# Optimization experiments

Hardware: AMD Instinct MI355X
Metric: run time of the kernel (lower is better)

Reference implementation:

```python
import jax, jax.numpy as jnp
import numpy as np

EPS = 1e-5  # torch LayerNorm default

def _layernorm(x, g, b):
    mu = jnp.mean(x, axis=-1, keepdims=True)
    var = jnp.mean(jnp.square(x - mu), axis=-1, keepdims=True)
    return (x - mu) * jax.lax.rsqrt(var + EPS) * g + b

def _gelu(x):
    return jax.nn.gelu(x, approximate=False)  # torch nn.GELU default is exact erf

def setup_inputs() -> dict:
    B, S, D, F = 2, 128, 64, 256
    key = jax.random.key(0)
    ks = jax.random.split(key, 8)
    def xavier(k, fan_in, fan_out, gain=1.0):
        lim = gain * np.sqrt(6.0 / (fan_in + fan_out))
        return jax.random.uniform(k, (fan_in, fan_out), jnp.float32, -lim, lim)
    return {
        "q": jax.random.normal(ks[0], (B, S, D), jnp.float32),
        # gauge generator MLP: Linear(2D, F) -> GELU -> Linear(F, D*D)
        "gw1": xavier(ks[1], 2 * D, F),
        "gb1": jnp.zeros((F,), jnp.float32),
        "gw2": xavier(ks[2], F, D * D, gain=0.01),  # nn.init.xavier_uniform_(gain=0.01)
        "gb2": jnp.zeros((D * D,), jnp.float32),    # nn.init.zeros_
        # block MLP: Linear(D, F) -> GELU -> Linear(F, D)
        "mw1": xavier(ks[3], D, F),
        "mb1": jnp.zeros((F,), jnp.float32),
        "mw2": xavier(ks[4], F, D),
        "mb2": jnp.zeros((D,), jnp.float32),
        # LayerNorms
        "ln1_g": jnp.ones((D,), jnp.float32),
        "ln1_b": jnp.zeros((D,), jnp.float32),
        "ln2_g": jnp.ones((D,), jnp.float32),
        "ln2_b": jnp.zeros((D,), jnp.float32),
    }

def reference(q, gw1, gb1, gw2, gb2, mw1, mb1, mw2, mb2, ln1_g, ln1_b, ln2_g, ln2_b):
    B, S, D = q.shape
    phi = q
    # pairwise features: cat(phi_i, phi_j) -> (B, S, S, 2D)
    phi_i = jnp.broadcast_to(phi[:, :, None, :], (B, S, S, D))
    phi_j = jnp.broadcast_to(phi[:, None, :, :], (B, S, S, D))
    pairs = jnp.concatenate([phi_i, phi_j], axis=-1)
    # gauge MLP -> U_ij in (B, S, S, D, D)
    h = _gelu(pairs @ gw1 + gb1)
    U = (h @ gw2 + gb2).reshape(B, S, S, D, D)
    # aggregate: sum_j U_ij @ phi_j  (contract d with phi feature dim)
    agg = jnp.einsum('bijde,bjd->bie', U, phi)
    # dropout in eval mode = identity
    phi = _layernorm(phi + agg, ln1_g, ln1_b)
    mlp_out = _gelu(phi @ mw1 + mb1) @ mw2 + mb2
    return _layernorm(phi + mlp_out, ln2_g, ln2_b)
```

## Files before the change

kernel.cpp:

```cpp
#include <hip/hip_runtime.h>
#include <hip/hip_bf16.h>
#include <math.h>

namespace {

constexpr int NB = 2, NS = 128, ND = 64, NF = 256;

typedef __attribute__((ext_vector_type(8))) short short8;
typedef __attribute__((ext_vector_type(8))) unsigned short ushort8;
typedef __attribute__((ext_vector_type(4))) float floatx4;

constexpr size_t OFF_W2   = 0;
constexpr size_t SZ_W2    = (size_t)NB * NS * NF * ND;
constexpr size_t OFF_P    = OFF_W2 + SZ_W2;
constexpr size_t SZ_P     = (size_t)NB * NS * NS * ND;
constexpr size_t OFF_AT   = OFF_P + SZ_P;
constexpr size_t SZ_AT    = (size_t)NB * NF * NS;
constexpr size_t OFF_BT   = OFF_AT + SZ_AT;
constexpr size_t SZ_BT    = (size_t)NB * NS * NF;
constexpr size_t OFF_BIAS = OFF_BT + SZ_BT;

__device__ __forceinline__ float gelu_fast(float x) {
  const float xs = fabsf(x) * 0.70710678118654752f;
  const float t = __builtin_amdgcn_rcpf(fmaf(0.3275911f, xs, 1.0f));
  float p = fmaf(1.061405429f, t, -1.453152027f);
  p = fmaf(p, t, 1.421413741f);
  p = fmaf(p, t, -0.284496736f);
  p = fmaf(p, t, 0.254829592f);
  p *= t;
  const float e = __expf(-xs * xs);
  const float erf_ax = fmaf(-p, e, 1.0f);
  const float erf_x = copysignf(erf_ax, x);
  return 0.5f * x * (1.0f + erf_x);
}

constexpr int QT_LD = NS + 4;

__global__ __launch_bounds__(256) void kA_pre(const float* __restrict__ q,
                                              const float* __restrict__ gw1,
                                              const float* __restrict__ gb1,
                                              const float* __restrict__ gw2,
                                              const float* __restrict__ gb2,
                                              float* __restrict__ A_t,
                                              float* __restrict__ Bt,
                                              float* __restrict__ W2,
                                              float* __restrict__ bias_agg) {
  __shared__ __align__(16) float smem[ND * QT_LD + ND * ND];
  const int t = threadIdx.x;
  const int bid = blockIdx.x;
  if (bid < NB * NS) {
    const int b = bid / NS, i = bid % NS;
    float* qrow = smem;
    if (t < ND) qrow[t] = q[((size_t)b * NS + i) * ND + t];
    __syncthreads();
    const int f = t;
    float a = 0.f, bb = gb1[f];
    #pragma unroll 8
    for (int d = 0; d < ND; ++d) {
      const float qd = qrow[d];
      a  += qd * gw1[d * NF + f];
      bb += qd * gw1[(ND + d) * NF + f];
    }
    A_t[((size_t)b * NF + f) * NS + i] = a;
    Bt[((size_t)b * NS + i) * NF + f] = bb;
  } else if (bid < NB * NS + NB * NF) {
    const int idx = bid - NB * NS;
    const int b = idx / NF, f = idx % NF;
    float* qt = smem;
    float* G  = smem + ND * QT_LD;
    for (int r = 0; r < ND * ND / 256; ++r)
      G[t + r * 256] = gw2[(size_t)f * ND * ND + t + r * 256];
    const float* qb = q + (size_t)b * NS * ND;
    for (int r = 0; r < NS * ND / 256; ++r) {
      const int lin = t + r * 256;
      const int j = lin >> 6, d = lin & 63;
      qt[d * QT_LD + j] = qb[lin];
    }
    __syncthreads();
    const int tj = t >> 3, te = t & 7;
    const int j0 = tj * 4, e0 = te * 8;
    float acc[4][8];
    #pragma unroll
    for (int jj = 0; jj < 4; ++jj)
      #pragma unroll
      for (int ee = 0; ee < 8; ++ee) acc[jj][ee] = 0.f;
    #pragma unroll 4
    for (int d = 0; d < ND; ++d) {
      const float4 qv = *(const float4*)&qt[d * QT_LD + j0];
      const float4 g0 = *(const float4*)&G[d * ND + e0];
      const float4 g1 = *(const float4*)&G[d * ND + e0 + 4];
      const float qa[4] = {qv.x, qv.y, qv.z, qv.w};
      const float ga[8] = {g0.x, g0.y, g0.z, g0.w, g1.x, g1.y, g1.z, g1.w};
      #pragma unroll
      for (int jj = 0; jj < 4; ++jj)
        #pragma unroll
        for (int ee = 0; ee < 8; ++ee) acc[jj][ee] += qa[jj] * ga[ee];
    }
    #pragma unroll
    for (int jj = 0; jj < 4; ++jj) {
      const int j = j0 + jj;
      float* dst = W2 + (((size_t)b * NS + j) * NF + f) * ND + e0;
      *(float4*)&dst[0] = make_float4(acc[jj][0], acc[jj][1], acc[jj][2], acc[jj][3]);
      *(float4*)&dst[4] = make_float4(acc[jj][4], acc[jj][5], acc[jj][6], acc[jj][7]);
    }
  } else {
    const int b = bid - (NB * NS + NB * NF);
    float* qs = smem;
    float* colsum = smem + NS * ND;
    const float* qb = q + (size_t)b * NS * ND;
    for (int r = 0; r < NS * ND / 256; ++r) qs[t + r * 256] = qb[t + r * 256];
    __syncthreads();
    if (t < ND) {
      float s = 0.f;
      for (int j = 0; j < NS; ++j) s += qs[j * ND + t];
      colsum[t] = s;
    }
    __syncthreads();
    if (t < ND) {
      float acc = 0.f;
      for (int d = 0; d < ND; ++d) acc += gb2[d * ND + t] * colsum[d];
      bias_agg[b * ND + t] = acc;
    }
  }
}

constexpr int HLD = 72;

__global__ __launch_bounds__(512) void k2_main(const float* __restrict__ A_t,
                                               const float* __restrict__ Bt,
                                               const float* __restrict__ W2,
                                               float* __restrict__ P) {
  const int b = blockIdx.x / NS, j = blockIdx.x % NS;
  const int t = threadIdx.x;
  const int lane = t & 63, w = t >> 6;
  __shared__ float Btj[NF];
  __shared__ __align__(16) unsigned short Hc[NS * HLD];
  __shared__ __align__(16) unsigned short Wc[ND * HLD];
  if (t < NF) Btj[t] = Bt[((size_t)b * NS + j) * NF + t];

  const float* W2bj = W2 + ((size_t)b * NS + j) * NF * ND;
  const float* Ab = A_t + (size_t)b * NF * NS;

  const int wi = (w & 3) * 32, we = (w >> 2) * 32;
  const int m = lane & 15, quad = lane >> 4;

  const int hi = (w & 1) * 64 + lane;
  const int hoct0 = t >> 7;
  const int weid = t & 63, woct = t >> 6;

  floatx4 acc[2][2];
  #pragma unroll
  for (int a0 = 0; a0 < 2; ++a0)
    #pragma unroll
    for (int a1 = 0; a1 < 2; ++a1) acc[a0][a1] = (floatx4)0.f;

  for (int c = 0; c < NF / 64; ++c) {
    __syncthreads();
    float wv[8];
    #pragma unroll
    for (int r = 0; r < 8; ++r)
      wv[r] = W2bj[(size_t)(c * 64 + woct * 8 + r) * ND + weid];
    float hv[2][8];
    #pragma unroll
    for (int s = 0; s < 2; ++s) {
      const int oct = hoct0 + 4 * s;
      #pragma unroll
      for (int r = 0; r < 8; ++r) {
        const int f = c * 64 + oct * 8 + r;
        hv[s][r] = gelu_fast(Ab[(size_t)f * NS + hi] + Btj[f]);
      }
    }
    {
      union { __hip_bfloat162 b2[4]; ushort8 v; } u;
      #pragma unroll
      for (int p = 0; p < 4; ++p)
        u.b2[p] = __float22bfloat162_rn(make_float2(wv[2 * p], wv[2 * p + 1]));
      *(ushort8*)&Wc[weid * HLD + woct * 8] = u.v;
    }
    #pragma unroll
    for (int s = 0; s < 2; ++s) {
      union { __hip_bfloat162 b2[4]; ushort8 v; } u;
      #pragma unroll
      for (int p = 0; p < 4; ++p)
        u.b2[p] = __float22bfloat162_rn(make_float2(hv[s][2 * p], hv[s][2 * p + 1]));
      *(ushort8*)&Hc[hi * HLD + (hoct0 + 4 * s) * 8] = u.v;
    }
    __syncthreads();
    #pragma unroll
    for (int kk = 0; kk < 2; ++kk) {
      short8 afr[2], bfr[2];
      #pragma unroll
      for (int ti = 0; ti < 2; ++ti)
        afr[ti] = *(const short8*)&Hc[(wi + ti * 16 + m) * HLD + kk * 32 + quad * 8];
      #pragma unroll
      for (int te = 0; te < 2; ++te)
        bfr[te] = *(const short8*)&Wc[(we + te * 16 + m) * HLD + kk * 32 + quad * 8];
      #pragma unroll
      for (int ti = 0; ti < 2; ++ti)
        #pragma unroll
        for (int te = 0; te < 2; ++te)
          acc[ti][te] = __builtin_amdgcn_mfma_f32_16x16x32_bf16(
              afr[ti], bfr[te], acc[ti][te], 0, 0, 0);
    }
  }
  float* Pbj = P + ((size_t)b * NS + j) * NS * ND;
  #pragma unroll
  for (int ti = 0; ti < 2; ++ti)
    #pragma unroll
    for (int te = 0; te < 2; ++te)
      #pragma unroll
      for (int r = 0; r < 4; ++r) {
        const int row = wi + ti * 16 + quad * 4 + r;
        const int col = we + te * 16 + m;
        Pbj[(size_t)row * ND + col] = acc[ti][te][r];
      }
}

__global__ __launch_bounds__(512) void k3_epi(const float* __restrict__ q,
                                              const float* __restrict__ P,
                                              const float* __restrict__ bias_agg,
                                              const float* __restrict__ mw1,
                                              const float* __restrict__ mb1,
                                              const float* __restrict__ mw2,
                                              const float* __restrict__ mb2,
                                              const float* __restrict__ ln1g,
                                              const float* __restrict__ ln1b,
                                              const float* __restrict__ ln2g,
                                              const float* __restrict__ ln2b,
                                              float* __restrict__ out) {
  const int b = blockIdx.x / NS, i = blockIdx.x % NS;
  const int t = threadIdx.x;
  const int e = t & 63, g = t >> 6;
  __shared__ float red[8 * ND];
  __shared__ float phi1[ND];
  __shared__ float hid[NF];
  const float* Pb = P + (size_t)b * NS * NS * ND;
  float s = 0.f;
  #pragma unroll 4
  for (int m0 = 0; m0 < 16; ++m0) {
    const int jj = g * 16 + m0;
    s += Pb[((size_t)jj * NS + i) * ND + e];
  }
  red[t] = s;
  __syncthreads();
  if (t < ND) {
    float agg = bias_agg[b * ND + e];
    #pragma unroll
    for (int gg = 0; gg < 8; ++gg) agg += red[gg * ND + e];
    const float x = q[((size_t)b * NS + i) * ND + e] + agg;
    float sum = x, sumsq = x * x;
    #pragma unroll
    for (int off = 32; off >= 1; off >>= 1) {
      sum += __shfl_xor(sum, off);
      sumsq += __shfl_xor(sumsq, off);
    }
    const float mu = sum * (1.f / 64.f);
    const float var = sumsq * (1.f / 64.f) - mu * mu;
    const float inv = rsqrtf(var + 1e-5f);
    phi1[e] = (x - mu) * inv * ln1g[e] + ln1b[e];
  }
  __syncthreads();
  if (t < NF) {
    float h = mb1[t];
    #pragma unroll 8
    for (int d = 0; d < ND; ++d) h += phi1[d] * mw1[d * NF + t];
    hid[t] = gelu_fast(h);
  }
  __syncthreads();
  {
    float p = 0.f;
    #pragma unroll 8
    for (int m0 = 0; m0 < 32; ++m0) {
      const int f = g * 32 + m0;
      p += hid[f] * mw2[f * ND + e];
    }
    red[t] = p;
  }
  __syncthreads();
  if (t < ND) {
    float mlp = mb2[e];
    #pragma unroll
    for (int gg = 0; gg < 8; ++gg) mlp += red[gg * ND + e];
    const float x = phi1[e] + mlp;
    float sum = x, sumsq = x * x;
    #pragma unroll
    for (int off = 32; off >= 1; off >>= 1) {
      sum += __shfl_xor(sum, off);
      sumsq += __shfl_xor(sumsq, off);
    }
    const float mu = sum * (1.f / 64.f);
    const float var = sumsq * (1.f / 64.f) - mu * mu;
    const float inv = rsqrtf(var + 1e-5f);
    out[((size_t)b * NS + i) * ND + e] = (x - mu) * inv * ln2g[e] + ln2b[e];
  }
}

}

extern "C" void kernel_launch(void* const* d_in, const int* in_sizes, int n_in,
                              void* d_out, int out_size, void* d_ws, size_t ws_size,
                              hipStream_t stream) {
  const float* q    = (const float*)d_in[0];
  const float* gw1  = (const float*)d_in[1];
  const float* gb1  = (const float*)d_in[2];
  const float* gw2  = (const float*)d_in[3];
  const float* gb2  = (const float*)d_in[4];
  const float* mw1  = (const float*)d_in[5];
  const float* mb1  = (const float*)d_in[6];
  const float* mw2  = (const float*)d_in[7];
  const float* mb2  = (const float*)d_in[8];
  const float* ln1g = (const float*)d_in[9];
  const float* ln1b = (const float*)d_in[10];
  const float* ln2g = (const float*)d_in[11];
  const float* ln2b = (const float*)d_in[12];
  float* out = (float*)d_out;
  float* ws  = (float*)d_ws;

  float* W2   = ws + OFF_W2;
  float* Pp   = ws + OFF_P;
  float* A_t  = ws + OFF_AT;
  float* Bt   = ws + OFF_BT;
  float* bias = ws + OFF_BIAS;

  kA_pre<<<NB * NS + NB * NF + NB, 256, 0, stream>>>(q, gw1, gb1, gw2, gb2,
                                                     A_t, Bt, W2, bias);
  k2_main<<<NB * NS, 512, 0, stream>>>(A_t, Bt, W2, Pp);
  k3_epi<<<NB * NS, 512, 0, stream>>>(q, Pp, bias, mw1, mb1, mw2, mb2,
                                      ln1g, ln1b, ln2g, ln2b, out);
}
```

Before: 112.9 us.

## Store W2 intermediate in bf16, compute it with MFMA, and prefetch in main loop

The precompute of W2 (q contracted with gw2 per feature) now runs on bf16 MFMA instructions with swizzled shared-memory tiles and writes a bf16 intermediate instead of fp32. That halves the global traffic for the largest workspace tensor, both on write and on read in the main kernel. The main kernel also register-prefetches the next chunk's W2 and A_t values before the barrier, so global loads overlap with compute, and the precompute blocks are regrouped with 512 threads each. The trade-off is an extra bf16 rounding of q and gw2 before the product is formed, plus scalar 2-byte output stores.

```diff
diff --git a/kernel.cpp b/kernel.cpp
--- a/kernel.cpp
+++ b/kernel.cpp
@@ -10,9 +10,9 @@
 typedef __attribute__((ext_vector_type(8))) unsigned short ushort8;
 typedef __attribute__((ext_vector_type(4))) float floatx4;
 
-constexpr size_t OFF_W2   = 0;
-constexpr size_t SZ_W2    = (size_t)NB * NS * NF * ND;
-constexpr size_t OFF_P    = OFF_W2 + SZ_W2;
+constexpr size_t OFF_W2H  = 0;
+constexpr size_t SZ_W2H   = (size_t)NB * NS * NF * ND / 2;
+constexpr size_t OFF_P    = OFF_W2H + SZ_W2H;
 constexpr size_t SZ_P     = (size_t)NB * NS * NS * ND;
 constexpr size_t OFF_AT   = OFF_P + SZ_P;
 constexpr size_t SZ_AT    = (size_t)NB * NF * NS;
@@ -34,92 +34,124 @@
   return 0.5f * x * (1.0f + erf_x);
 }
 
-constexpr int QT_LD = NS + 4;
-
-__global__ __launch_bounds__(256) void kA_pre(const float* __restrict__ q,
+__device__ __forceinline__ ushort8 pack_bf16x8(const float v[8]) {
+  union { __hip_bfloat162 b2[4]; ushort8 u; } u;
+  #pragma unroll
+  for (int p = 0; p < 4; ++p)
+    u.b2[p] = __float22bfloat162_rn(make_float2(v[2 * p], v[2 * p + 1]));
+  return u.u;
+}
+
+__global__ __launch_bounds__(512) void kA_pre(const float* __restrict__ q,
                                               const float* __restrict__ gw1,
                                               const float* __restrict__ gb1,
                                               const float* __restrict__ gw2,
                                               const float* __restrict__ gb2,
                                               float* __restrict__ A_t,
                                               float* __restrict__ Bt,
-                                              float* __restrict__ W2,
+                                              unsigned short* __restrict__ W2h,
                                               float* __restrict__ bias_agg) {
-  __shared__ __align__(16) float smem[ND * QT_LD + ND * ND];
-  const int t = threadIdx.x;
-  const int bid = blockIdx.x;
-  if (bid < NB * NS) {
-    const int b = bid / NS, i = bid % NS;
-    float* qrow = smem;
-    if (t < ND) qrow[t] = q[((size_t)b * NS + i) * ND + t];
+  __shared__ __align__(16) unsigned short smem_u[128 * 64 + 8 * 64 * 40];
+  float* smf = (float*)smem_u;
+  const int t = threadIdx.x, bid = blockIdx.x;
+
+  if (bid < 128) {
+    const int b = bid >> 6, ip = bid & 63;
+    const int half = t >> 8, f = t & 255;
+    const int i = ip * 2 + half;
+    float* qrow = smf;
+    if (f < 64) qrow[half * 64 + f] = q[((size_t)b * NS + i) * ND + f];
     __syncthreads();
-    const int f = t;
     float a = 0.f, bb = gb1[f];
     #pragma unroll 8
     for (int d = 0; d < ND; ++d) {
-      const float qd = qrow[d];
+      const float qd = qrow[half * 64 + d];
       a  += qd * gw1[d * NF + f];
       bb += qd * gw1[(ND + d) * NF + f];
     }
     A_t[((size_t)b * NF + f) * NS + i] = a;
     Bt[((size_t)b * NS + i) * NF + f] = bb;
-  } else if (bid < NB * NS + NB * NF) {
-    const int idx = bid - NB * NS;
-    const int b = idx / NF, f = idx % NF;
-    float* qt = smem;
-    float* G  = smem + ND * QT_LD;
-    for (int r = 0; r < ND * ND / 256; ++r)
-      G[t + r * 256] = gw2[(size_t)f * ND * ND + t + r * 256];
-    const float* qb = q + (size_t)b * NS * ND;
-    for (int r = 0; r < NS * ND / 256; ++r) {
-      const int lin = t + r * 256;
-      const int j = lin >> 6, d = lin & 63;
-      qt[d * QT_LD + j] = qb[lin];
-    }
-    __syncthreads();
-    const int tj = t >> 3, te = t & 7;
-    const int j0 = tj * 4, e0 = te * 8;
-    float acc[4][8];
-    #pragma unroll
-    for (int jj = 0; jj < 4; ++jj)
-      #pragma unroll
-      for (int ee = 0; ee < 8; ++ee) acc[jj][ee] = 0.f;
-    #pragma unroll 4
-    for (int d = 0; d < ND; ++d) {
-      const float4 qv = *(const float4*)&qt[d * QT_LD + j0];
-      const float4 g0 = *(const float4*)&G[d * ND + e0];
-      const float4 g1 = *(const float4*)&G[d * ND + e0 + 4];
-      const float qa[4] = {qv.x, qv.y, qv.z, qv.w};
-      const float ga[8] = {g0.x, g0.y, g0.z, g0.w, g1.x, g1.y, g1.z, g1.w};
-      #pragma unroll
-      for (int jj = 0; jj < 4; ++jj)
-        #pragma unroll
-        for (int ee = 0; ee < 8; ++ee) acc[jj][ee] += qa[jj] * ga[ee];
-    }
-    #pragma unroll
-    for (int jj = 0; jj < 4; ++jj) {
-      const int j = j0 + jj;
-      float* dst = W2 + (((size_t)b * NS + j) * NF + f) * ND + e0;
-      *(float4*)&dst[0] = make_float4(acc[jj][0], acc[jj][1], acc[jj][2], acc[jj][3]);
-      *(float4*)&dst[4] = make_float4(acc[jj][4], acc[jj][5], acc[jj][6], acc[jj][7]);
-    }
+  } else if (bid < 192) {
+    const int idx = bid - 128;
+    const int b = idx >> 5, f0 = (idx & 31) * 8;
+    unsigned short* qbf = smem_u;
+    unsigned short* Gt  = smem_u + 128 * 64;
+    {
+      const int jq = t >> 1, half = t & 1;
+      const float* src = q + ((size_t)b * NS + jq) * ND + half * 32;
+      #pragma unroll
+      for (int p = 0; p < 4; ++p) {
+        float v[8];
+        #pragma unroll
+        for (int r = 0; r < 8; ++r) v[r] = src[p * 8 + r];
+        const int oct = half * 4 + p;
+        const int col = oct ^ (jq & 7);
+        *(ushort8*)&qbf[jq * 64 + col * 8] = pack_bf16x8(v);
+      }
+    }
+    const int lane = t & 63, w = t >> 6;
+    const int f = f0 + w;
+    const int m = lane & 15, quad = lane >> 4;
+    const int te = t & 63, tf = t >> 6;
+    floatx4 acc[8][4];
+    #pragma unroll
+    for (int ti = 0; ti < 8; ++ti)
+      #pragma unroll
+      for (int tn = 0; tn < 4; ++tn) acc[ti][tn] = (floatx4)0.f;
+
+    for (int dc = 0; dc < 2; ++dc) {
+      __syncthreads();
+      const float* gsrc = gw2 + (size_t)(f0 + tf) * (ND * ND) + (size_t)(dc * 32) * ND + te;
+      #pragma unroll
+      for (int p = 0; p < 4; ++p) {
+        float gv[8];
+        #pragma unroll
+        for (int r = 0; r < 8; ++r) gv[r] = gsrc[(size_t)(p * 8 + r) * ND];
+        *(ushort8*)&Gt[tf * 2560 + te * 40 + p * 8] = pack_bf16x8(gv);
+      }
+      __syncthreads();
+      short8 bfr[4];
+      #pragma unroll
+      for (int tn = 0; tn < 4; ++tn)
+        bfr[tn] = *(const short8*)&Gt[w * 2560 + (tn * 16 + m) * 40 + quad * 8];
+      #pragma unroll
+      for (int ti = 0; ti < 8; ++ti) {
+        const int jr = ti * 16 + m;
+        const int col = (dc * 4 + quad) ^ (jr & 7);
+        const short8 afr = *(const short8*)&qbf[jr * 64 + col * 8];
+        #pragma unroll
+        for (int tn = 0; tn < 4; ++tn)
+          acc[ti][tn] = __builtin_amdgcn_mfma_f32_16x16x32_bf16(afr, bfr[tn],
+                                                                acc[ti][tn], 0, 0, 0);
+      }
+    }
+    __hip_bfloat16* Wh = (__hip_bfloat16*)W2h;
+    #pragma unroll
+    for (int ti = 0; ti < 8; ++ti)
+      #pragma unroll
+      for (int r = 0; r < 4; ++r) {
+        const int jr = ti * 16 + quad * 4 + r;
+        __hip_bfloat16* dst = Wh + ((size_t)(b * NS + jr) * NF + f) * ND;
+        #pragma unroll
+        for (int tn = 0; tn < 4; ++tn)
+          dst[tn * 16 + m] = __float2bfloat16(acc[ti][tn][r]);
+      }
   } else {
-    const int b = bid - (NB * NS + NB * NF);
-    float* qs = smem;
-    float* colsum = smem + NS * ND;
-    const float* qb = q + (size_t)b * NS * ND;
-    for (int r = 0; r < NS * ND / 256; ++r) qs[t + r * 256] = qb[t + r * 256];
+    const int b = bid - 192;
+    float* qs = smf;
+    float* colsum = smf + NS * ND;
+    for (int r = 0; r < 16; ++r) qs[t + r * 512] = q[(size_t)b * NS * ND + t + r * 512];
     __syncthreads();
     if (t < ND) {
       float s = 0.f;
-      for (int j = 0; j < NS; ++j) s += qs[j * ND + t];
+      for (int jj = 0; jj < NS; ++jj) s += qs[jj * ND + t];
       colsum[t] = s;
     }
     __syncthreads();
     if (t < ND) {
-      float acc = 0.f;
-      for (int d = 0; d < ND; ++d) acc += gb2[d * ND + t] * colsum[d];
-      bias_agg[b * ND + t] = acc;
+      float a2 = 0.f;
+      for (int d = 0; d < ND; ++d) a2 += gb2[d * ND + t] * colsum[d];
+      bias_agg[b * ND + t] = a2;
     }
   }
 }
@@ -128,7 +160,7 @@
 
 __global__ __launch_bounds__(512) void k2_main(const float* __restrict__ A_t,
                                                const float* __restrict__ Bt,
-                                               const float* __restrict__ W2,
+                                               const unsigned short* __restrict__ W2h,
                                                float* __restrict__ P) {
   const int b = blockIdx.x / NS, j = blockIdx.x % NS;
   const int t = threadIdx.x;
@@ -138,15 +170,13 @@
   __shared__ __align__(16) unsigned short Wc[ND * HLD];
   if (t < NF) Btj[t] = Bt[((size_t)b * NS + j) * NF + t];
 
-  const float* W2bj = W2 + ((size_t)b * NS + j) * NF * ND;
+  const unsigned short* Whbj = W2h + (size_t)(b * NS + j) * NF * ND;
   const float* Ab = A_t + (size_t)b * NF * NS;
 
   const int wi = (w & 3) * 32, we = (w >> 2) * 32;
   const int m = lane & 15, quad = lane >> 4;
-
-  const int hi = (w & 1) * 64 + lane;
-  const int hoct0 = t >> 7;
-  const int weid = t & 63, woct = t >> 6;
+  const int hi = (w & 1) * 64 + lane, hoct0 = w >> 1;
+  const int wei = t & 63, woct = w;
 
   floatx4 acc[2][2];
   #pragma unroll
@@ -154,36 +184,46 @@
     #pragma unroll
     for (int a1 = 0; a1 < 2; ++a1) acc[a0][a1] = (floatx4)0.f;
 
+  unsigned short wvv[8];
+  #pragma unroll
+  for (int r = 0; r < 8; ++r)
+    wvv[r] = Whbj[(size_t)(woct * 8 + r) * ND + wei];
+  float ar[2][8];
+  #pragma unroll
+  for (int s = 0; s < 2; ++s)
+    #pragma unroll
+    for (int r = 0; r < 8; ++r)
+      ar[s][r] = Ab[(size_t)((hoct0 + 4 * s) * 8 + r) * NS + hi];
+  __syncthreads();
+
   for (int c = 0; c < NF / 64; ++c) {
-    __syncthreads();
-    float wv[8];
-    #pragma unroll
-    for (int r = 0; r < 8; ++r)
-      wv[r] = W2bj[(size_t)(c * 64 + woct * 8 + r) * ND + weid];
-    float hv[2][8];
+    ushort8 hv[2];
     #pragma unroll
     for (int s = 0; s < 2; ++s) {
-      const int oct = hoct0 + 4 * s;
+      float hvf[8];
       #pragma unroll
       for (int r = 0; r < 8; ++r) {
-        const int f = c * 64 + oct * 8 + r;
-        hv[s][r] = gelu_fast(Ab[(size_t)f * NS + hi] + Btj[f]);
-      }
-    }
-    {
-      union { __hip_bfloat162 b2[4]; ushort8 v; } u;
-      #pragma unroll
-      for (int p = 0; p < 4; ++p)
-        u.b2[p] = __float22bfloat162_rn(make_float2(wv[2 * p], wv[2 * p + 1]));
-      *(ushort8*)&Wc[weid * HLD + woct * 8] = u.v;
-    }
-    #pragma unroll
-    for (int s = 0; s < 2; ++s) {
-      union { __hip_bfloat162 b2[4]; ushort8 v; } u;
-      #pragma unroll
-      for (int p = 0; p < 4; ++p)
-        u.b2[p] = __float22bfloat162_rn(make_float2(hv[s][2 * p], hv[s][2 * p + 1]));
-      *(ushort8*)&Hc[hi * HLD + (hoct0 + 4 * s) * 8] = u.v;
+        const int fl = c * 64 + (hoct0 + 4 * s) * 8 + r;
+        hvf[r] = gelu_fast(ar[s][r] + Btj[fl]);
+      }
+      hv[s] = pack_bf16x8(hvf);
+    }
+    union { unsigned short a[8]; ushort8 v; } wu;
+    #pragma unroll
+    for (int r = 0; r < 8; ++r) wu.a[r] = wvv[r];
+    if (c > 0) __syncthreads();
+    *(ushort8*)&Wc[wei * HLD + woct * 8] = wu.v;
+    *(ushort8*)&Hc[hi * HLD + hoct0 * 8] = hv[0];
+    *(ushort8*)&Hc[hi * HLD + (hoct0 + 4) * 8] = hv[1];
+    if (c < NF / 64 - 1) {
+      #pragma unroll
+      for (int r = 0; r < 8; ++r)
+        wvv[r] = Whbj[(size_t)((c + 1) * 64 + woct * 8 + r) * ND + wei];
+      #pragma unroll
+      for (int s = 0; s < 2; ++s)
+        #pragma unroll
+        for (int r = 0; r < 8; ++r)
+          ar[s][r] = Ab[(size_t)((c + 1) * 64 + (hoct0 + 4 * s) * 8 + r) * NS + hi];
     }
     __syncthreads();
     #pragma unroll
@@ -316,15 +356,14 @@
   float* out = (float*)d_out;
   float* ws  = (float*)d_ws;
 
-  float* W2   = ws + OFF_W2;
+  unsigned short* W2h = (unsigned short*)(ws + OFF_W2H);
   float* Pp   = ws + OFF_P;
   float* A_t  = ws + OFF_AT;
   float* Bt   = ws + OFF_BT;
   float* bias = ws + OFF_BIAS;
 
-  kA_pre<<<NB * NS + NB * NF + NB, 256, 0, stream>>>(q, gw1, gb1, gw2, gb2,
-                                                     A_t, Bt, W2, bias);
-  k2_main<<<NB * NS, 512, 0, stream>>>(A_t, Bt, W2, Pp);
+  kA_pre<<<194, 512, 0, stream>>>(q, gw1, gb1, gw2, gb2, A_t, Bt, W2h, bias);
+  k2_main<<<NB * NS, 512, 0, stream>>>(A_t, Bt, W2h, Pp);
   k3_epi<<<NB * NS, 512, 0, stream>>>(q, Pp, bias, mw1, mb1, mw2, mb2,
                                       ln1g, ln1b, ln2g, ln2b, out);
 }
```

New measurement: 109.4 us. 3.1% less time.
